# Optimization experiments

Hardware: AMD Instinct MI355X
Metric: run time of the kernel (lower is better)

Reference implementation:

```python
import jax, jax.numpy as jnp
import numpy as np

OMEGA = 1.5

def _sine(x, W, b, omega=OMEGA):
    return jnp.sin(omega * (x @ W.T + b))

def setup_inputs() -> dict:
    key = jax.random.key(0)
    ks = jax.random.split(key, 17)
    I = J = K = 384
    mid, R = 256, 100
    s = 0.05  # small init scale, mimics uniform(-1/in, 1/in) style init
    return {
        "A_input": jax.random.normal(ks[0], (I, 1), jnp.float32),
        "B_input": jax.random.normal(ks[1], (J, 1), jnp.float32),
        "C_input": jax.random.normal(ks[2], (K, 1), jnp.float32),
        "A_W1": jax.random.normal(ks[3], (mid, 1), jnp.float32) * s,
        "A_b1": jax.random.normal(ks[4], (mid,), jnp.float32) * s,
        "A_W2": jax.random.normal(ks[5], (R, mid), jnp.float32) * s,
        "A_b2": jax.random.normal(ks[6], (R,), jnp.float32) * s,
        "B_W1": jax.random.normal(ks[7], (mid, 1), jnp.float32) * s,
        "B_b1": jax.random.normal(ks[8], (mid,), jnp.float32) * s,
        "B_W2": jax.random.normal(ks[9], (R, mid), jnp.float32) * s,
        "B_b2": jax.random.normal(ks[10], (R,), jnp.float32) * s,
        "C_W1": jax.random.normal(ks[11], (mid, 1), jnp.float32) * s,
        "C_b1": jax.random.normal(ks[12], (mid,), jnp.float32) * s,
        "C_W2": jax.random.normal(ks[13], (mid, mid), jnp.float32) * s,
        "C_b2": jax.random.normal(ks[14], (mid,), jnp.float32) * s,
        "C_W3": jax.random.normal(ks[15], (R, mid), jnp.float32) * s,
        "C_b3": jax.random.normal(ks[16], (R,), jnp.float32) * s,
    }

def reference(A_input, B_input, C_input,
              A_W1, A_b1, A_W2, A_b2,
              B_W1, B_b1, B_W2, B_b2,
              C_W1, C_b1, C_W2, C_b2, C_W3, C_b3):
    # Factor networks
    A = _sine(A_input, A_W1, A_b1) @ A_W2.T + A_b2                  # [I, R]
    B = _sine(B_input, B_W1, B_b1) @ B_W2.T + B_b2                  # [J, R]
    C = _sine(_sine(C_input, C_W1, C_b1), C_W2, C_b2) @ C_W3.T + C_b3  # [K, R]
    # The frozen core is super-diagonal (core[r,r,r]=1), so the permute/matmul
    # chain reduces exactly to the CP contraction sum_r A[i,r]*B[j,r]*C[k,r].
    return jnp.einsum('ir,jr,kr->ijk', A, B, C)  # [I, J, K]
```

## Files before the change

kernel.cpp:

```cpp
#include <hip/hip_runtime.h>
#include <hip/hip_bf16.h>

#define RR 100
#define MID 256
#define NN 384
#define KP 128

typedef __attribute__((ext_vector_type(8))) __bf16 bf16x8;
typedef __attribute__((ext_vector_type(4))) float floatx4;
typedef unsigned short ushort_t;

#define SW(row, ch) ((((row) << 7)) + ((((ch) ^ ((row) & 15))) << 3))

__device__ __forceinline__ ushort_t f2bf(float f) {
  __hip_bfloat16 h = __float2bfloat16(f);
  return __builtin_bit_cast(ushort_t, h);
}

__global__ __launch_bounds__(256) void factors_kernel(
    const float* __restrict__ xA, const float* __restrict__ xB,
    const float* __restrict__ xC,
    const float* __restrict__ AW1, const float* __restrict__ Ab1,
    const float* __restrict__ AW2, const float* __restrict__ Ab2,
    const float* __restrict__ BW1, const float* __restrict__ Bb1,
    const float* __restrict__ BW2, const float* __restrict__ Bb2,
    const float* __restrict__ CW1, const float* __restrict__ Cb1,
    const float* __restrict__ CW2, const float* __restrict__ Cb2,
    const float* __restrict__ CW3, const float* __restrict__ Cb3,
    float* __restrict__ Af, float* __restrict__ Bf,
    ushort_t* __restrict__ Cbf) {
  __shared__ float h[MID];
  __shared__ float h2[MID];
  const int i = blockIdx.x;
  const int net = blockIdx.y;
  const int t = threadIdx.x;

  const float* x  = (net == 0) ? xA  : (net == 1) ? xB  : xC;
  const float* W1 = (net == 0) ? AW1 : (net == 1) ? BW1 : CW1;
  const float* b1 = (net == 0) ? Ab1 : (net == 1) ? Bb1 : Cb1;

  const float xv = x[i];
  h[t] = sinf(1.5f * (xv * W1[t] + b1[t]));
  __syncthreads();

  const float* hlast = h;
  if (net == 2) {
    float acc = Cb2[t];
    const float* __restrict__ w = &CW2[t * MID];
#pragma unroll 8
    for (int m = 0; m < MID; ++m) acc += h[m] * w[m];
    h2[t] = sinf(1.5f * acc);
    __syncthreads();
    hlast = h2;
  }

  const float* W2 = (net == 0) ? AW2 : (net == 1) ? BW2 : CW3;
  const float* b2 = (net == 0) ? Ab2 : (net == 1) ? Bb2 : Cb3;

  if (t < KP) {
    float v = 0.0f;
    if (t < RR) {
      float acc = b2[t];
      const float* __restrict__ w = &W2[t * MID];
#pragma unroll 8
      for (int m = 0; m < MID; ++m) acc += hlast[m] * w[m];
      v = acc;
    }
    if (net == 0)      Af[i * KP + t] = v;
    else if (net == 1) Bf[i * KP + t] = v;
    else               Cbf[i * KP + t] = f2bf(v);
  }
}

__global__ __launch_bounds__(256, 2) void cp_mfma(
    const float* __restrict__ Af, const float* __restrict__ Bf,
    const ushort_t* __restrict__ Cbf, float* __restrict__ out) {
  __shared__ ushort_t Wt[128 * KP];
  __shared__ ushort_t Ct[128 * KP];

  const int i  = blockIdx.z;
  const int j0 = blockIdx.y * 128;
  const int k0 = blockIdx.x * 128;
  const int t  = threadIdx.x;

#pragma unroll
  for (int it = 0; it < 8; ++it) {
    const int idx = t + 256 * it;
    const int row = idx >> 4;
    const int ch  = idx & 15;
    *(uint4*)&Ct[SW(row, ch)] =
        *(const uint4*)&Cbf[(size_t)(k0 + row) * KP + ch * 8];
  }

  {
    const int jx = t >> 1;
    const int hh = t & 1;
    const float* __restrict__ arow = Af + (size_t)i * KP + hh * 64;
    const float* __restrict__ brow = Bf + (size_t)(j0 + jx) * KP + hh * 64;
#pragma unroll
    for (int c = 0; c < 8; ++c) {
      const float4 a0 = *(const float4*)(arow + c * 8);
      const float4 a1 = *(const float4*)(arow + c * 8 + 4);
      const float4 b0 = *(const float4*)(brow + c * 8);
      const float4 b1 = *(const float4*)(brow + c * 8 + 4);
      uint4 wv;
      wv.x = (unsigned)f2bf(a0.x * b0.x) | ((unsigned)f2bf(a0.y * b0.y) << 16);
      wv.y = (unsigned)f2bf(a0.z * b0.z) | ((unsigned)f2bf(a0.w * b0.w) << 16);
      wv.z = (unsigned)f2bf(a1.x * b1.x) | ((unsigned)f2bf(a1.y * b1.y) << 16);
      wv.w = (unsigned)f2bf(a1.z * b1.z) | ((unsigned)f2bf(a1.w * b1.w) << 16);
      *(uint4*)&Wt[SW(jx, hh * 8 + c)] = wv;
    }
  }
  __syncthreads();

  const int lane = t & 63;
  const int w    = t >> 6;
  const int wj   = (w & 1) * 64;
  const int wk   = (w >> 1) * 64;
  const int m16  = lane & 15;
  const int g    = lane >> 4;

  floatx4 acc[4][4];
#pragma unroll
  for (int jf = 0; jf < 4; ++jf)
#pragma unroll
    for (int kf = 0; kf < 4; ++kf) acc[jf][kf] = (floatx4)0.0f;

#pragma unroll
  for (int ks = 0; ks < 4; ++ks) {
    bf16x8 af[4], bfr[4];
#pragma unroll
    for (int f = 0; f < 4; ++f) {
      af[f]  = *(const bf16x8*)&Wt[SW(wj + f * 16 + m16, ks * 4 + g)];
      bfr[f] = *(const bf16x8*)&Ct[SW(wk + f * 16 + m16, ks * 4 + g)];
    }
#pragma unroll
    for (int jf = 0; jf < 4; ++jf)
#pragma unroll
      for (int kf = 0; kf < 4; ++kf)
        acc[jf][kf] = __builtin_amdgcn_mfma_f32_16x16x32_bf16(
            af[jf], bfr[kf], acc[jf][kf], 0, 0, 0);
  }

  const size_t ibase = (size_t)i * NN * NN;
#pragma unroll
  for (int jf = 0; jf < 4; ++jf) {
    const int j = j0 + wj + jf * 16 + g * 4;
#pragma unroll
    for (int kf = 0; kf < 4; ++kf) {
      const int k = k0 + wk + kf * 16 + m16;
#pragma unroll
      for (int r = 0; r < 4; ++r) {
        out[ibase + (size_t)(j + r) * NN + k] = acc[jf][kf][r];
      }
    }
  }
}

extern "C" void kernel_launch(void* const* d_in, const int* in_sizes, int n_in,
                              void* d_out, int out_size, void* d_ws, size_t ws_size,
                              hipStream_t stream) {
  const float* A_input = (const float*)d_in[0];
  const float* B_input = (const float*)d_in[1];
  const float* C_input = (const float*)d_in[2];
  const float* A_W1 = (const float*)d_in[3];
  const float* A_b1 = (const float*)d_in[4];
  const float* A_W2 = (const float*)d_in[5];
  const float* A_b2 = (const float*)d_in[6];
  const float* B_W1 = (const float*)d_in[7];
  const float* B_b1 = (const float*)d_in[8];
  const float* B_W2 = (const float*)d_in[9];
  const float* B_b2 = (const float*)d_in[10];
  const float* C_W1 = (const float*)d_in[11];
  const float* C_b1 = (const float*)d_in[12];
  const float* C_W2 = (const float*)d_in[13];
  const float* C_b2 = (const float*)d_in[14];
  const float* C_W3 = (const float*)d_in[15];
  const float* C_b3 = (const float*)d_in[16];

  float* Af = (float*)d_ws;
  float* Bf = Af + NN * KP;
  ushort_t* Cbf = (ushort_t*)(Bf + NN * KP);

  dim3 fgrid(NN, 3);
  factors_kernel<<<fgrid, 256, 0, stream>>>(
      A_input, B_input, C_input,
      A_W1, A_b1, A_W2, A_b2,
      B_W1, B_b1, B_W2, B_b2,
      C_W1, C_b1, C_W2, C_b2, C_W3, C_b3,
      Af, Bf, Cbf);

  dim3 grid(NN / 128, NN / 128, NN);
  cp_mfma<<<grid, 256, 0, stream>>>(Af, Bf, Cbf, (float*)d_out);
}
```

Baseline: 298.6 us.

## Drop LDS staging in CP kernel, load fragments from global, store float4 nontemporal

The CP contraction kernel no longer stages the A*B product and C tiles in shared memory. Each wave loads its MFMA fragments straight from global/L2 and forms the bf16 A*B products in registers. The MFMA operands are swapped so each lane holds four consecutive k values, which allows 16-byte nontemporal float4 stores of the output instead of scalar stores. Launch bounds are raised to three blocks per CU, and the factor MLP dot products are vectorised with float4 loads. This removes LDS traffic and barriers and improves write coalescing on a store-bound output, at the cost of redundant global loads and recomputing the A*B products per wave.

```diff
diff --git a/kernel.cpp b/kernel.cpp
--- a/kernel.cpp
+++ b/kernel.cpp
@@ -9,8 +9,6 @@
 typedef __attribute__((ext_vector_type(8))) __bf16 bf16x8;
 typedef __attribute__((ext_vector_type(4))) float floatx4;
 typedef unsigned short ushort_t;
-
-#define SW(row, ch) ((((row) << 7)) + ((((ch) ^ ((row) & 15))) << 3))
 
 __device__ __forceinline__ ushort_t f2bf(float f) {
   __hip_bfloat16 h = __float2bfloat16(f);
@@ -47,8 +45,15 @@
   if (net == 2) {
     float acc = Cb2[t];
     const float* __restrict__ w = &CW2[t * MID];
-#pragma unroll 8
-    for (int m = 0; m < MID; ++m) acc += h[m] * w[m];
+#pragma unroll 4
+    for (int m = 0; m < MID; m += 4) {
+      const float4 wv = *(const float4*)&w[m];
+      const float4 hv = *(const float4*)&h[m];
+      acc += hv.x * wv.x;
+      acc += hv.y * wv.y;
+      acc += hv.z * wv.z;
+      acc += hv.w * wv.w;
+    }
     h2[t] = sinf(1.5f * acc);
     __syncthreads();
     hlast = h2;
@@ -62,8 +67,15 @@
     if (t < RR) {
       float acc = b2[t];
       const float* __restrict__ w = &W2[t * MID];
-#pragma unroll 8
-      for (int m = 0; m < MID; ++m) acc += hlast[m] * w[m];
+#pragma unroll 4
+      for (int m = 0; m < MID; m += 4) {
+        const float4 wv = *(const float4*)&w[m];
+        const float4 hv = *(const float4*)&hlast[m];
+        acc += hv.x * wv.x;
+        acc += hv.y * wv.y;
+        acc += hv.z * wv.z;
+        acc += hv.w * wv.w;
+      }
       v = acc;
     }
     if (net == 0)      Af[i * KP + t] = v;
@@ -72,46 +84,13 @@
   }
 }
 
-__global__ __launch_bounds__(256, 2) void cp_mfma(
+__global__ __launch_bounds__(256, 3) void cp_mfma(
     const float* __restrict__ Af, const float* __restrict__ Bf,
     const ushort_t* __restrict__ Cbf, float* __restrict__ out) {
-  __shared__ ushort_t Wt[128 * KP];
-  __shared__ ushort_t Ct[128 * KP];
-
   const int i  = blockIdx.z;
   const int j0 = blockIdx.y * 128;
   const int k0 = blockIdx.x * 128;
   const int t  = threadIdx.x;
-
-#pragma unroll
-  for (int it = 0; it < 8; ++it) {
-    const int idx = t + 256 * it;
-    const int row = idx >> 4;
-    const int ch  = idx & 15;
-    *(uint4*)&Ct[SW(row, ch)] =
-        *(const uint4*)&Cbf[(size_t)(k0 + row) * KP + ch * 8];
-  }
-
-  {
-    const int jx = t >> 1;
-    const int hh = t & 1;
-    const float* __restrict__ arow = Af + (size_t)i * KP + hh * 64;
-    const float* __restrict__ brow = Bf + (size_t)(j0 + jx) * KP + hh * 64;
-#pragma unroll
-    for (int c = 0; c < 8; ++c) {
-      const float4 a0 = *(const float4*)(arow + c * 8);
-      const float4 a1 = *(const float4*)(arow + c * 8 + 4);
-      const float4 b0 = *(const float4*)(brow + c * 8);
-      const float4 b1 = *(const float4*)(brow + c * 8 + 4);
-      uint4 wv;
-      wv.x = (unsigned)f2bf(a0.x * b0.x) | ((unsigned)f2bf(a0.y * b0.y) << 16);
-      wv.y = (unsigned)f2bf(a0.z * b0.z) | ((unsigned)f2bf(a0.w * b0.w) << 16);
-      wv.z = (unsigned)f2bf(a1.x * b1.x) | ((unsigned)f2bf(a1.y * b1.y) << 16);
-      wv.w = (unsigned)f2bf(a1.z * b1.z) | ((unsigned)f2bf(a1.w * b1.w) << 16);
-      *(uint4*)&Wt[SW(jx, hh * 8 + c)] = wv;
-    }
-  }
-  __syncthreads();
 
   const int lane = t & 63;
   const int w    = t >> 6;
@@ -122,37 +101,51 @@
 
   floatx4 acc[4][4];
 #pragma unroll
-  for (int jf = 0; jf < 4; ++jf)
+  for (int kf = 0; kf < 4; ++kf)
 #pragma unroll
-    for (int kf = 0; kf < 4; ++kf) acc[jf][kf] = (floatx4)0.0f;
+    for (int jf = 0; jf < 4; ++jf) acc[kf][jf] = (floatx4)0.0f;
+
+  const float* __restrict__ arow = Af + (size_t)i * KP;
 
 #pragma unroll
   for (int ks = 0; ks < 4; ++ks) {
-    bf16x8 af[4], bfr[4];
+    const int rc = (ks * 4 + g) * 8;
+
+    const float4 a0 = *(const float4*)(arow + rc);
+    const float4 a1 = *(const float4*)(arow + rc + 4);
+
+    bf16x8 cf[4];
 #pragma unroll
-    for (int f = 0; f < 4; ++f) {
-      af[f]  = *(const bf16x8*)&Wt[SW(wj + f * 16 + m16, ks * 4 + g)];
-      bfr[f] = *(const bf16x8*)&Ct[SW(wk + f * 16 + m16, ks * 4 + g)];
-    }
+    for (int kf = 0; kf < 4; ++kf)
+      cf[kf] = *(const bf16x8*)&Cbf[(size_t)(k0 + wk + kf * 16 + m16) * KP + rc];
+
 #pragma unroll
-    for (int jf = 0; jf < 4; ++jf)
+    for (int jf = 0; jf < 4; ++jf) {
+      const float* __restrict__ brow =
+          Bf + (size_t)(j0 + wj + jf * 16 + m16) * KP + rc;
+      const float4 b0 = *(const float4*)(brow);
+      const float4 b1 = *(const float4*)(brow + 4);
+      union { unsigned u[4]; bf16x8 v; } wf;
+      wf.u[0] = (unsigned)f2bf(a0.x * b0.x) | ((unsigned)f2bf(a0.y * b0.y) << 16);
+      wf.u[1] = (unsigned)f2bf(a0.z * b0.z) | ((unsigned)f2bf(a0.w * b0.w) << 16);
+      wf.u[2] = (unsigned)f2bf(a1.x * b1.x) | ((unsigned)f2bf(a1.y * b1.y) << 16);
+      wf.u[3] = (unsigned)f2bf(a1.z * b1.z) | ((unsigned)f2bf(a1.w * b1.w) << 16);
 #pragma unroll
       for (int kf = 0; kf < 4; ++kf)
-        acc[jf][kf] = __builtin_amdgcn_mfma_f32_16x16x32_bf16(
-            af[jf], bfr[kf], acc[jf][kf], 0, 0, 0);
+        acc[kf][jf] = __builtin_amdgcn_mfma_f32_16x16x32_bf16(
+            cf[kf], wf.v, acc[kf][jf], 0, 0, 0);
+    }
   }
 
   const size_t ibase = (size_t)i * NN * NN;
 #pragma unroll
-  for (int jf = 0; jf < 4; ++jf) {
-    const int j = j0 + wj + jf * 16 + g * 4;
+  for (int kf = 0; kf < 4; ++kf) {
+    const int k = k0 + wk + kf * 16 + g * 4;
 #pragma unroll
-    for (int kf = 0; kf < 4; ++kf) {
-      const int k = k0 + wk + kf * 16 + m16;
-#pragma unroll
-      for (int r = 0; r < 4; ++r) {
-        out[ibase + (size_t)(j + r) * NN + k] = acc[jf][kf][r];
-      }
+    for (int jf = 0; jf < 4; ++jf) {
+      const int j = j0 + wj + jf * 16 + m16;
+      __builtin_nontemporal_store(
+          acc[kf][jf], (floatx4*)&out[ibase + (size_t)j * NN + k]);
     }
   }
 }
```

After: 356.0 us. 19.2% more time.
